# Performance work log

Measured on AMD Instinct MI355X. Metric: run time of the kernel, lower is better.

## Reference

```python
import jax, jax.numpy as jnp
import numpy as np

CH = [344, 352, 686, 679, 1246, 973]  # int(128*3*0.8984), etc.


def binarize(x):
    # sign forward, hardtanh STE backward (standard 1W1A binarization)
    cl = jnp.clip(x, -1.0, 1.0)
    return cl + jax.lax.stop_gradient(jnp.sign(x) - cl)


def bconv(x, w):
    # BinarizeConv2d: conv(sign(x), sign(w)), 3x3, stride 1, pad 1, no bias
    return jax.lax.conv_general_dilated(
        binarize(x), binarize(w), (1, 1), ((1, 1), (1, 1)),
        dimension_numbers=("NCHW", "OIHW", "NCHW"))


def bn(x, p, eps=1e-5):
    # p: [4, C] stacked (gamma, beta, running_mean, running_var), inference BN
    g, b, m, v = p[0], p[1], p[2], p[3]
    scale = (g * jax.lax.rsqrt(v + eps))[None, :, None, None]
    return (x - m[None, :, None, None]) * scale + b[None, :, None, None]


def pool(x):
    return jax.lax.reduce_window(x, -jnp.inf, jax.lax.max,
                                 (1, 1, 2, 2), (1, 1, 2, 2), "VALID")


def htanh(x):
    return jnp.clip(x, -1.0, 1.0)


def setup_inputs() -> dict:
    key = jax.random.key(0)
    ks = jax.random.split(key, 20)
    x = jax.random.normal(ks[0], (256, 3, 32, 32), jnp.float32)
    chs = [3] + CH
    out = {"x": x}
    for i in range(6):
        n = 3 * 3 * chs[i + 1]
        w = jax.random.normal(ks[1 + i], (chs[i + 1], chs[i], 3, 3), jnp.float32) * np.sqrt(2.0 / n).astype(np.float32)
        out[f"w{i}"] = w
        g = jnp.ones((chs[i + 1],), jnp.float32)
        b = jnp.zeros((chs[i + 1],), jnp.float32)
        m = jax.random.normal(ks[7 + i], (chs[i + 1],), jnp.float32) * 0.1
        v = jax.random.uniform(ks[13 + i], (chs[i + 1],), jnp.float32) * 0.5 + 0.5
        out[f"p{i}"] = jnp.stack([g, b, m, v])
    out["fcw"] = jax.random.normal(ks[19], (10, 15568), jnp.float32) * 0.01
    out["fcb"] = jnp.zeros((10,), jnp.float32)
    return out


def reference(x, w0, w1, w2, w3, w4, w5, p0, p1, p2, p3, p4, p5, fcw, fcb):
    x = htanh(bn(bconv(x, w0), p0))          # [B,344,32,32]
    x = htanh(bn(pool(bconv(x, w1)), p1))    # [B,352,16,16]
    x = htanh(bn(bconv(x, w2), p2))          # [B,686,16,16]
    x = htanh(bn(pool(bconv(x, w3)), p3))    # [B,679,8,8]
    x = htanh(bn(bconv(x, w4), p4))          # [B,1246,8,8]
    x = htanh(bn(pool(bconv(x, w5)), p5))    # [B,973,4,4]
    x = x.reshape(x.shape[0], -1)            # [B,15568]
    return binarize(x) @ binarize(fcw).T + fcb
```

## Files before the change

kernel.cpp:

```cpp
#include <hip/hip_runtime.h>
#include <stdint.h>

typedef unsigned long long u64;
typedef int v4i  __attribute__((ext_vector_type(4)));
typedef int v8i  __attribute__((ext_vector_type(8)));
typedef float v16f __attribute__((ext_vector_type(16)));

static __device__ __forceinline__ v16f mfma_fp4(v4i a, v4i b, v16f c) {
    v8i A, B;
    A[0] = a[0]; A[1] = a[1]; A[2] = a[2]; A[3] = a[3];
    A[4] = a[0]; A[5] = a[1]; A[6] = a[2]; A[7] = a[3];
    B[0] = b[0]; B[1] = b[1]; B[2] = b[2]; B[3] = b[3];
    B[4] = b[0]; B[5] = b[1]; B[6] = b[2]; B[7] = b[3];
    return __builtin_amdgcn_mfma_scale_f32_32x32x64_f8f6f4(
        A, B, c, 4, 4, 0, 0x7F7F7F7F, 0, 0x7F7F7F7F);
}

static __device__ __forceinline__ void gload_lds16(const void* g, void* l) {
    __builtin_amdgcn_global_load_lds(
        (const __attribute__((address_space(1))) unsigned int*)g,
        (__attribute__((address_space(3))) unsigned int*)l, 16, 0, 0);
}

__global__ void pack_input_kernel(const float* __restrict__ x, u64* __restrict__ a0)
{
    int idx = blockIdx.x * blockDim.x + threadIdx.x;
    if (idx >= 256 * 1024) return;
    int b = idx >> 10, pix = idx & 1023;
    const float* xp = x + (size_t)b * 3072 + pix;
    u64 wd = 0;
    if (xp[0]    > 0.f) wd |= 1ull;
    if (xp[1024] > 0.f) wd |= 2ull;
    if (xp[2048] > 0.f) wd |= 4ull;
    a0[idx] = wd;
}

__global__ void pack_w_fp4(const float* __restrict__ w, unsigned* __restrict__ wb,
                           int O, int C, int KWIN, int OCG)
{
    int idx = blockIdx.x * blockDim.x + threadIdx.x;
    int total = 9 * KWIN * OCG * 64;
    if (idx >= total) return;
    int lane = idx & 63;
    int rest = idx >> 6;
    int og = rest % OCG; rest /= OCG;
    int c64 = rest % KWIN; int t = rest / KWIN;
    int oc = og * 32 + (lane & 31);
    int h = lane >> 5;
    unsigned out[4];
#pragma unroll
    for (int d = 0; d < 4; ++d) {
        unsigned dw = 0;
#pragma unroll
        for (int j = 0; j < 8; ++j) {
            int c = c64 * 64 + h * 32 + d * 8 + ((j >> 1) + (j & 1) * 4);
            unsigned nib = 0;
            if (oc < O && c < C)
                nib = (w[(size_t)(oc * C + c) * 9 + t] > 0.f) ? 0x2u : 0xAu;
            dw |= nib << (4 * j);
        }
        out[d] = dw;
    }
    *(v4i*)(wb + (size_t)idx * 4) = *(v4i*)out;
}

__global__ void pack_bn_kernel(const float* __restrict__ p, float* __restrict__ sa,
                               float* __restrict__ sb, int C)
{
    int i = blockIdx.x * blockDim.x + threadIdx.x;
    if (i >= C) return;
    float g = p[i], b = p[C + i], m = p[2 * C + i], v = p[3 * C + i];
    float s = g * rsqrtf(v + 1e-5f);
    sa[i] = s;
    sb[i] = fmaf(-m, s, b);
}

__global__ void pack_fc_kernel(const float* __restrict__ fcw, u64* __restrict__ wfc)
{
    int idx = blockIdx.x * blockDim.x + threadIdx.x;
    if (idx >= 10 * 256) return;
    int w = idx & 15;
    int p = (idx >> 4) & 15;
    int k = idx >> 8;
    u64 word = 0;
    for (int c2 = 0; c2 < 64; ++c2) {
        int c = w * 64 + c2;
        if (c < 973) {
            if (fcw[(size_t)k * 15568 + c * 16 + p] > 0.f) word |= (1ull << c2);
        }
    }
    wfc[idx] = word;
}

static __device__ __forceinline__ v4i fp4_unpack32(unsigned wh)
{
    v4i r;
#pragma unroll
    for (int d = 0; d < 4; ++d) {
        unsigned b = (wh >> (8 * d)) & 0xffu;
        unsigned lo = ((b & 0xFu) * 0x00204081u) & 0x01010101u;
        unsigned hi = ((b >> 4)   * 0x00204081u) & 0x01010101u;
        unsigned spread = lo | (hi << 4);
        r[d] = (int)(0xAAAAAAAAu - (spread << 3));
    }
    return r;
}

template <int H, int W, int TH, int TW, int NIMG, int KWIN, int OCG_T, int OCW,
          int COUT, bool POOL>
__global__ __launch_bounds__(256, 2)
void conv_v6f(const u64* __restrict__ act, const char* __restrict__ wb,
              const float* __restrict__ sA, const float* __restrict__ sB,
              u64* __restrict__ outp)
{
    constexpr int CW = TW + 2;
    constexpr int CELLS_I = (TH + 2) * CW;
    constexpr int CELLS = NIMG * CELLS_I;
    constexpr int PLANE = CELLS * 16;
    constexpr int BSZ = 18432;
    __shared__ __attribute__((aligned(16))) char smem[BSZ + 2 * PLANE];

    const int tid  = threadIdx.x;
    const int lane = tid & 63;
    const int wm   = tid >> 6;
    const int h    = lane >> 5;
    const int m    = lane & 31;

    int b0i, y0;
    if constexpr (NIMG == 1) {
        b0i = blockIdx.x >> 1;
        y0 = (blockIdx.x & 1) * TH;
    } else {
        b0i = blockIdx.x * NIMG;
        y0 = 0;
    }

    const int ocg0 = blockIdx.y * 2;
    const int gw   = blockIdx.y;

    int aoff[4];
#pragma unroll
    for (int ag = 0; ag < 4; ++ag) {
        int p = wm * 128 + ag * 32 + m;
        int img = p / (TH * TW);
        int pp = p % (TH * TW);
        aoff[ag] = ((img * CELLS_I + (pp / TW) * CW + (pp % TW)) << 4) + h * PLANE;
    }

    v16f acc[4][2];
#pragma unroll
    for (int ag = 0; ag < 4; ++ag)
#pragma unroll
        for (int o = 0; o < 2; ++o)
#pragma unroll
            for (int i = 0; i < 16; ++i) acc[ag][o][i] = 0.0f;

#pragma unroll 1
    for (int c64 = 0; c64 < KWIN; ++c64) {
        for (int u = wm; u < 18; u += 4) {
            int og = u & 1, t = u >> 1;
            const char* gp = wb + ((size_t)((t * KWIN + c64) * OCG_T + ocg0 + og)) * 1024
                             + lane * 16;
            gload_lds16(gp, smem + u * 1024);
        }
        for (int cell = tid; cell < CELLS; cell += 256) {
            int img, c2;
            if constexpr (NIMG == 1) { img = 0; c2 = cell; }
            else { img = cell / CELLS_I; c2 = cell % CELLS_I; }
            int cy = c2 / CW, cx = c2 % CW;
            int gy = y0 + cy - 1, gx = cx - 1;
            char* dst = smem + BSZ + cell * 16;
            if ((unsigned)gy < (unsigned)H && (unsigned)gx < (unsigned)W) {
                u64 wd = act[((size_t)(b0i + img) * H * W + (size_t)gy * W + gx) * KWIN + c64];
                *(v4i*)dst           = fp4_unpack32((unsigned)wd);
                *(v4i*)(dst + PLANE) = fp4_unpack32((unsigned)(wd >> 32));
            } else {
                v4i z = {0, 0, 0, 0};
                *(v4i*)dst           = z;
                *(v4i*)(dst + PLANE) = z;
            }
        }
        __syncthreads();

#pragma unroll
        for (int t = 0; t < 9; ++t) {
            const int aimm = BSZ + (((t / 3) * CW) + (t % 3)) * 16;
            v4i b0 = *(const v4i*)(smem + (t * 2 + 0) * 1024 + lane * 16);
            v4i b1 = *(const v4i*)(smem + (t * 2 + 1) * 1024 + lane * 16);
            v4i a0 = *(const v4i*)(smem + aoff[0] + aimm);
            v4i a1 = *(const v4i*)(smem + aoff[1] + aimm);
            v4i a2 = *(const v4i*)(smem + aoff[2] + aimm);
            v4i a3 = *(const v4i*)(smem + aoff[3] + aimm);
            acc[0][0] = mfma_fp4(a0, b0, acc[0][0]);
            acc[1][0] = mfma_fp4(a1, b0, acc[1][0]);
            acc[2][0] = mfma_fp4(a2, b0, acc[2][0]);
            acc[3][0] = mfma_fp4(a3, b0, acc[3][0]);
            acc[0][1] = mfma_fp4(a0, b1, acc[0][1]);
            acc[1][1] = mfma_fp4(a1, b1, acc[1][1]);
            acc[2][1] = mfma_fp4(a2, b1, acc[2][1]);
            acc[3][1] = mfma_fp4(a3, b1, acc[3][1]);
        }
        __syncthreads();
    }

    const int ocA = ocg0 * 32 + m;
    const int ocB = ocA + 32;
    const float fa0 = sA[ocA < COUT ? ocA : 0], fb0 = sB[ocA < COUT ? ocA : 0];
    const float fa1 = sA[ocB < COUT ? ocB : 0], fb1 = sB[ocB < COUT ? ocB : 0];

#pragma unroll
    for (int ag = 0; ag < 4; ++ag) {
        if constexpr (POOL && TW == 32) {
            if (ag & 1) continue;
#pragma unroll
            for (int gi = 0; gi < 8; ++gi) {
                const int g = gi * 2;
                float v0 = fmaxf(fmaxf(acc[ag][0][g], acc[ag][0][g ^ 1]),
                                 fmaxf(acc[ag + 1][0][g], acc[ag + 1][0][g ^ 1]));
                float v1 = fmaxf(fmaxf(acc[ag][1][g], acc[ag][1][g ^ 1]),
                                 fmaxf(acc[ag + 1][1][g], acc[ag + 1][1][g ^ 1]));
                u64 bal0 = __ballot((ocA < COUT) && (fmaf(v0, fa0, fb0) > 0.f));
                u64 bal1 = __ballot((ocB < COUT) && (fmaf(v1, fa1, fb1) > 0.f));
                u64 w_lo = (bal0 & 0xffffffffull) | (bal1 << 32);
                u64 w_hi = (bal0 >> 32) | (bal1 & 0xffffffff00000000ull);
                int pyo  = wm * 2 + (ag >> 1);
                int pxo0 = ((g & 3) >> 1) + 4 * (g >> 2);
                size_t rowb = ((size_t)b0i * (H / 2) + (y0 / 2 + pyo)) * (W / 2);
                if (lane == (ag >> 1) * 16 + gi * 2)
                    outp[(rowb + pxo0) * OCW + gw] = w_lo;
                else if (lane == (ag >> 1) * 16 + gi * 2 + 1)
                    outp[(rowb + pxo0 + 2) * OCW + gw] = w_hi;
            }
        } else if constexpr (POOL) {
#pragma unroll
            for (int gi = 0; gi < 4; ++gi) {
                const int g = gi * 2;
                float v0 = fmaxf(fmaxf(acc[ag][0][g], acc[ag][0][g ^ 1]),
                                 fmaxf(acc[ag][0][g ^ 8], acc[ag][0][(g ^ 8) | 1]));
                float v1 = fmaxf(fmaxf(acc[ag][1][g], acc[ag][1][g ^ 1]),
                                 fmaxf(acc[ag][1][g ^ 8], acc[ag][1][(g ^ 8) | 1]));
                u64 bal0 = __ballot((ocA < COUT) && (fmaf(v0, fa0, fb0) > 0.f));
                u64 bal1 = __ballot((ocB < COUT) && (fmaf(v1, fa1, fb1) > 0.f));
                u64 w_lo = (bal0 & 0xffffffffull) | (bal1 << 32);
                u64 w_hi = (bal0 >> 32) | (bal1 & 0xffffffff00000000ull);
                int img  = wm >> 1;
                int pyo  = (wm & 1) * 4 + ag;
                int pxo0 = ((g >> 1) & 1) | (((g >> 2) & 1) << 2);
                size_t rowb = ((size_t)(b0i + img) * (TH / 2) + pyo) * (TW / 2);
                if (lane == (ag * 4 + gi) * 2)
                    outp[(rowb + pxo0) * OCW + gw] = w_lo;
                else if (lane == (ag * 4 + gi) * 2 + 1)
                    outp[(rowb + pxo0 + 2) * OCW + gw] = w_hi;
            }
        } else {
#pragma unroll
            for (int reg = 0; reg < 16; ++reg) {
                u64 bal0 = __ballot((ocA < COUT) && (fmaf(acc[ag][0][reg], fa0, fb0) > 0.f));
                u64 bal1 = __ballot((ocB < COUT) && (fmaf(acc[ag][1][reg], fa1, fb1) > 0.f));
                u64 w_lo = (bal0 & 0xffffffffull) | (bal1 << 32);
                u64 w_hi = (bal0 >> 32) | (bal1 & 0xffffffff00000000ull);
                int row  = (reg & 3) + 8 * (reg >> 2);
                int p_lo = wm * 128 + ag * 32 + row;
                int p_hi = p_lo + 4;
                if (lane == reg * 2) {
                    int img, py, px;
                    if constexpr (TW == 32) { img = 0; py = p_lo >> 5; px = p_lo & 31; }
                    else { img = p_lo >> 8; py = (p_lo >> 4) & 15; px = p_lo & 15; }
                    outp[(((size_t)(b0i + img) * H + (y0 + py)) * W + px) * OCW + gw] = w_lo;
                } else if (lane == reg * 2 + 1) {
                    int img, py, px;
                    if constexpr (TW == 32) { img = 0; py = p_hi >> 5; px = p_hi & 31; }
                    else { img = p_hi >> 8; py = (p_hi >> 4) & 15; px = p_hi & 15; }
                    outp[(((size_t)(b0i + img) * H + (y0 + py)) * W + px) * OCW + gw] = w_hi;
                }
            }
        }
    }
}

template <int KWIN, int OCG, int OCW, int COUT, bool POOL>
__global__ __launch_bounds__(256, 3)
void conv_m8f(const u64* __restrict__ act, const char* __restrict__ wb,
              const float* __restrict__ sA, const float* __restrict__ sB,
              u64* __restrict__ outp)
{
    constexpr int CELLS = 100;
    constexpr int PLANE = CELLS * 16;
    constexpr int IMG = 2 * PLANE;
    __shared__ __attribute__((aligned(16))) char smem[4 * IMG];

    const int tid  = threadIdx.x;
    const int lane = tid & 63;
    const int wave = tid >> 6;
    const int h    = lane >> 5;
    const int m    = lane & 31;

    const int b = blockIdx.x * 4 + wave;
    const int ocg0 = blockIdx.y * 2;
    const int gw = blockIdx.y;

    int aoff[2];
#pragma unroll
    for (int ph = 0; ph < 2; ++ph) {
        int p = ph * 32 + m;
        aoff[ph] = wave * IMG + ((p >> 3) * 10 + (p & 7)) * 16 + h * PLANE;
    }

    v16f acc[2][2];
#pragma unroll
    for (int a = 0; a < 2; ++a)
#pragma unroll
        for (int o = 0; o < 2; ++o)
#pragma unroll
            for (int i = 0; i < 16; ++i) acc[a][o][i] = 0.0f;

    const u64* actb = act + (size_t)b * (64 * KWIN);

    v4i b0n, b1n;
    {
        const v4i* pn = (const v4i*)(wb + ((size_t)ocg0) * 1024) + lane;
        b0n = pn[0]; b1n = pn[64];
    }

#pragma unroll 1
    for (int c64 = 0; c64 < KWIN; ++c64) {
        for (int cell = lane; cell < CELLS; cell += 64) {
            int cy = cell / 10, cx = cell % 10;
            int gy = cy - 1, gx = cx - 1;
            char* dst = smem + wave * IMG + cell * 16;
            if ((unsigned)gy < 8u && (unsigned)gx < 8u) {
                u64 wd = actb[((size_t)gy * 8 + gx) * KWIN + c64];
                *(v4i*)dst           = fp4_unpack32((unsigned)wd);
                *(v4i*)(dst + PLANE) = fp4_unpack32((unsigned)(wd >> 32));
            } else {
                v4i z = {0, 0, 0, 0};
                *(v4i*)dst           = z;
                *(v4i*)(dst + PLANE) = z;
            }
        }
        __syncthreads();

#pragma unroll
        for (int t = 0; t < 9; ++t) {
            v4i b0 = b0n, b1 = b1n;
            {
                const int tn = (t + 1) % 9;
                const int cn = (t == 8) ? (c64 + 1) : c64;
                const v4i* pn = (const v4i*)(wb + ((size_t)((tn * KWIN + cn) * OCG + ocg0)) * 1024) + lane;
                b0n = pn[0]; b1n = pn[64];
            }
            const int toff = ((t / 3) * 10 + (t % 3)) * 16;
            v4i a0 = *(const v4i*)(smem + aoff[0] + toff);
            v4i a1 = *(const v4i*)(smem + aoff[1] + toff);
            acc[0][0] = mfma_fp4(a0, b0, acc[0][0]);
            acc[1][0] = mfma_fp4(a1, b0, acc[1][0]);
            acc[0][1] = mfma_fp4(a0, b1, acc[0][1]);
            acc[1][1] = mfma_fp4(a1, b1, acc[1][1]);
        }
        __syncthreads();
    }

    const int ocA = ocg0 * 32 + m;
    const int ocB = ocA + 32;
    const float fa0 = sA[ocA < COUT ? ocA : 0], fb0 = sB[ocA < COUT ? ocA : 0];
    const float fa1 = sA[ocB < COUT ? ocB : 0], fb1 = sB[ocB < COUT ? ocB : 0];

#pragma unroll
    for (int ph = 0; ph < 2; ++ph) {
        if constexpr (POOL) {
#pragma unroll
            for (int gi = 0; gi < 4; ++gi) {
                const int g = (gi & 1) * 2 + (gi >> 1) * 8;
                float v0 = fmaxf(fmaxf(acc[ph][0][g], acc[ph][0][g ^ 1]),
                                 fmaxf(acc[ph][0][g ^ 4], acc[ph][0][(g ^ 4) | 1]));
                float v1 = fmaxf(fmaxf(acc[ph][1][g], acc[ph][1][g ^ 1]),
                                 fmaxf(acc[ph][1][g ^ 4], acc[ph][1][(g ^ 4) | 1]));
                u64 bal0 = __ballot((ocA < COUT) && (fmaf(v0, fa0, fb0) > 0.f));
                u64 bal1 = __ballot((ocB < COUT) && (fmaf(v1, fa1, fb1) > 0.f));
                u64 w_lo = (bal0 & 0xffffffffull) | (bal1 << 32);
                u64 w_hi = (bal0 >> 32) | (bal1 & 0xffffffff00000000ull);
                int pyo  = ph * 2 + ((g >> 3) & 1);
                int pxo0 = (g >> 1) & 1;
                int pxo1 = pxo0 | 2;
                size_t rowb = ((size_t)b * 4 + pyo) * 4;
                if (lane == (ph * 4 + gi) * 2)
                    outp[(rowb + pxo0) * OCW + gw] = w_lo;
                else if (lane == (ph * 4 + gi) * 2 + 1)
                    outp[(rowb + pxo1) * OCW + gw] = w_hi;
            }
        } else {
#pragma unroll
            for (int reg = 0; reg < 16; ++reg) {
                u64 bal0 = __ballot((ocA < COUT) && (fmaf(acc[ph][0][reg], fa0, fb0) > 0.f));
                u64 bal1 = __ballot((ocB < COUT) && (fmaf(acc[ph][1][reg], fa1, fb1) > 0.f));
                u64 w_lo = (bal0 & 0xffffffffull) | (bal1 << 32);
                u64 w_hi = (bal0 >> 32) | (bal1 & 0xffffffff00000000ull);
                int row  = (reg & 3) + 8 * (reg >> 2);
                int p_lo = ph * 32 + row;
                int p_hi = p_lo + 4;
                if (lane == reg * 2)
                    outp[(((size_t)b * 8 + (p_lo >> 3)) * 8 + (p_lo & 7)) * OCW + gw] = w_lo;
                else if (lane == reg * 2 + 1)
                    outp[(((size_t)b * 8 + (p_hi >> 3)) * 8 + (p_hi & 7)) * OCW + gw] = w_hi;
            }
        }
    }
}

__global__ void fc_kernel(const u64* __restrict__ a6, const u64* __restrict__ wfc,
                          const float* __restrict__ fcb, float* __restrict__ out)
{
    int idx = blockIdx.x * blockDim.x + threadIdx.x;
    if (idx >= 2560) return;
    int k = idx % 10, b = idx / 10;
    const u64* ap = a6 + (size_t)b * 256;
    const u64* wq = wfc + (size_t)k * 256;
    int pop = 0;
#pragma unroll 8
    for (int q = 0; q < 256; ++q) pop += __popcll(ap[q] ^ wq[q]);
    out[idx] = (float)(15568 - 2 * pop) + fcb[k];
}

extern "C" void kernel_launch(void* const* d_in, const int* in_sizes, int n_in,
                              void* d_out, int out_size, void* d_ws, size_t ws_size,
                              hipStream_t stream)
{
    const float* x   = (const float*)d_in[0];
    const float* w0  = (const float*)d_in[1];
    const float* p0  = (const float*)d_in[2];
    const float* w1  = (const float*)d_in[3];
    const float* p1  = (const float*)d_in[4];
    const float* w2  = (const float*)d_in[5];
    const float* p2  = (const float*)d_in[6];
    const float* w3  = (const float*)d_in[7];
    const float* p3  = (const float*)d_in[8];
    const float* w4  = (const float*)d_in[9];
    const float* p4  = (const float*)d_in[10];
    const float* w5  = (const float*)d_in[11];
    const float* p5  = (const float*)d_in[12];
    const float* fcw = (const float*)d_in[13];
    const float* fcb = (const float*)d_in[14];
    float* out = (float*)d_out;

    u64* WS = (u64*)d_ws;
    u64* A0 = WS;
    u64* A1 = A0 + 262144;
    u64* A2 = A1 + 1572864;
    u64* A3 = A2 + 393216;
    u64* A4 = A3 + 720896;
    u64* A5 = A4 + 180224;
    u64* A6 = A5 + 327680;
    u64* WFp = A6 + 65536;
    char* WB0 = (char*)(WFp + 2560);
    char* WB1 = WB0 + 110592;
    char* WB2 = WB1 + 663552;
    char* WB3 = WB2 + 1327104;
    char* WB4 = WB3 + 2433024;
    char* WB5 = WB4 + 4055040;
    float* SA0 = (float*)(WB5 + 5898240);
    float* SB0 = SA0 + 1280;
    float* SA1 = SB0 + 1280;
    float* SB1 = SA1 + 1280;
    float* SA2 = SB1 + 1280;
    float* SB2 = SA2 + 1280;
    float* SA3 = SB2 + 1280;
    float* SB3 = SA3 + 1280;
    float* SA4 = SB3 + 1280;
    float* SB4 = SA4 + 1280;
    float* SA5 = SB4 + 1280;
    float* SB5 = SA5 + 1280;

    pack_input_kernel<<<1024, 256, 0, stream>>>(x, A0);
    pack_w_fp4<<<(9 * 1 * 12 * 64 + 255) / 256, 256, 0, stream>>>(w0, (unsigned*)WB0, 344, 3, 1, 12);
    pack_w_fp4<<<(9 * 6 * 12 * 64 + 255) / 256, 256, 0, stream>>>(w1, (unsigned*)WB1, 352, 344, 6, 12);
    pack_w_fp4<<<(9 * 6 * 24 * 64 + 255) / 256, 256, 0, stream>>>(w2, (unsigned*)WB2, 686, 352, 6, 24);
    pack_w_fp4<<<(9 * 11 * 24 * 64 + 255) / 256, 256, 0, stream>>>(w3, (unsigned*)WB3, 679, 686, 11, 24);
    pack_w_fp4<<<(9 * 11 * 40 * 64 + 255) / 256, 256, 0, stream>>>(w4, (unsigned*)WB4, 1246, 679, 11, 40);
    pack_w_fp4<<<(9 * 20 * 32 * 64 + 255) / 256, 256, 0, stream>>>(w5, (unsigned*)WB5, 973, 1246, 20, 32);
    pack_bn_kernel<<<2, 256, 0, stream>>>(p0, SA0, SB0, 344);
    pack_bn_kernel<<<2, 256, 0, stream>>>(p1, SA1, SB1, 352);
    pack_bn_kernel<<<3, 256, 0, stream>>>(p2, SA2, SB2, 686);
    pack_bn_kernel<<<3, 256, 0, stream>>>(p3, SA3, SB3, 679);
    pack_bn_kernel<<<5, 256, 0, stream>>>(p4, SA4, SB4, 1246);
    pack_bn_kernel<<<4, 256, 0, stream>>>(p5, SA5, SB5, 973);
    pack_fc_kernel<<<10, 256, 0, stream>>>(fcw, WFp);

    conv_v6f<32, 32, 16, 32, 1,  1, 12,  6, 344, false>
        <<<dim3(512, 6), 256, 0, stream>>>(A0, WB0, SA0, SB0, A1);
    conv_v6f<32, 32, 16, 32, 1,  6, 12,  6, 352, true>
        <<<dim3(512, 6), 256, 0, stream>>>(A1, WB1, SA1, SB1, A2);
    conv_v6f<16, 16, 16, 16, 2,  6, 24, 11, 686, false>
        <<<dim3(128, 11), 256, 0, stream>>>(A2, WB2, SA2, SB2, A3);
    conv_v6f<16, 16, 16, 16, 2, 11, 24, 11, 679, true>
        <<<dim3(128, 11), 256, 0, stream>>>(A3, WB3, SA3, SB3, A4);
    conv_m8f<11, 40, 20, 1246, false>
        <<<dim3(64, 20), 256, 0, stream>>>(A4, WB4, SA4, SB4, A5);
    conv_m8f<20, 32, 16, 973, true>
        <<<dim3(64, 16), 256, 0, stream>>>(A5, WB5, SA5, SB5, A6);

    fc_kernel<<<10, 256, 0, stream>>>(A6, WFp, fcb, out);
}
```

Baseline: 971.3 us.

## Double-buffer conv tiles and prefetch next channel chunk during MFMA loop

The main conv kernel now keeps two LDS buffers. During the MFMA loop over the current 64-channel chunk it prefetches the next chunk's weights, via global_load_lds, and its activation words into registers. Cell addresses and zero padding are computed once up front, and one of the two block barriers per iteration is removed. The 8x8 per-wave kernel drops its block barriers and uses wave-local lgkmcnt waits, with register prefetch of the next chunk's activations. The cost is twice the LDS for the main kernel, which may lower occupancy, and a risk of wave-level races in the per-wave kernel.

After: 3.088 ms. +218.0%, slower.

```diff
diff --git a/kernel.cpp b/kernel.cpp
--- a/kernel.cpp
+++ b/kernel.cpp
@@ -118,7 +118,10 @@
     constexpr int CELLS = NIMG * CELLS_I;
     constexpr int PLANE = CELLS * 16;
     constexpr int BSZ = 18432;
-    __shared__ __attribute__((aligned(16))) char smem[BSZ + 2 * PLANE];
+    constexpr int BUF = BSZ + 2 * PLANE;
+    constexpr int NBUF = (KWIN > 1) ? 2 : 1;
+    constexpr int NCELL = (CELLS + 255) / 256;
+    __shared__ __attribute__((aligned(16))) char smem[NBUF * BUF];
 
     const int tid  = threadIdx.x;
     const int lane = tid & 63;
@@ -147,50 +150,98 @@
         aoff[ag] = ((img * CELLS_I + (pp / TW) * CW + (pp % TW)) << 4) + h * PLANE;
     }
 
-    v16f acc[4][2];
-#pragma unroll
-    for (int ag = 0; ag < 4; ++ag)
-#pragma unroll
-        for (int o = 0; o < 2; ++o)
-#pragma unroll
-            for (int i = 0; i < 16; ++i) acc[ag][o][i] = 0.0f;
-
-#pragma unroll 1
-    for (int c64 = 0; c64 < KWIN; ++c64) {
-        for (int u = wm; u < 18; u += 4) {
-            int og = u & 1, t = u >> 1;
-            const char* gp = wb + ((size_t)((t * KWIN + c64) * OCG_T + ocg0 + og)) * 1024
-                             + lane * 16;
-            gload_lds16(gp, smem + u * 1024);
-        }
-        for (int cell = tid; cell < CELLS; cell += 256) {
+    const u64* cp[NCELL];
+    int  coff[NCELL];
+    bool cval[NCELL];
+#pragma unroll
+    for (int i = 0; i < NCELL; ++i) {
+        cval[i] = false; cp[i] = act; coff[i] = 0;
+        int cell = tid + i * 256;
+        if (cell < CELLS) {
             int img, c2;
             if constexpr (NIMG == 1) { img = 0; c2 = cell; }
             else { img = cell / CELLS_I; c2 = cell % CELLS_I; }
             int cy = c2 / CW, cx = c2 % CW;
             int gy = y0 + cy - 1, gx = cx - 1;
-            char* dst = smem + BSZ + cell * 16;
+            coff[i] = cell * 16;
             if ((unsigned)gy < (unsigned)H && (unsigned)gx < (unsigned)W) {
-                u64 wd = act[((size_t)(b0i + img) * H * W + (size_t)gy * W + gx) * KWIN + c64];
-                *(v4i*)dst           = fp4_unpack32((unsigned)wd);
-                *(v4i*)(dst + PLANE) = fp4_unpack32((unsigned)(wd >> 32));
+                cval[i] = true;
+                cp[i] = act + ((size_t)(b0i + img) * H * W + (size_t)gy * W + gx) * KWIN;
             } else {
                 v4i z = {0, 0, 0, 0};
-                *(v4i*)dst           = z;
-                *(v4i*)(dst + PLANE) = z;
-            }
-        }
-        __syncthreads();
+                *(v4i*)(smem + BSZ + cell * 16)         = z;
+                *(v4i*)(smem + BSZ + cell * 16 + PLANE) = z;
+                if constexpr (NBUF == 2) {
+                    *(v4i*)(smem + BUF + BSZ + cell * 16)         = z;
+                    *(v4i*)(smem + BUF + BSZ + cell * 16 + PLANE) = z;
+                }
+            }
+        }
+    }
+
+    const char* bsrc[5];
+#pragma unroll
+    for (int k = 0; k < 5; ++k) {
+        const int u = wm + 4 * k;
+        if (u < 18) {
+            const int og = u & 1, t = u >> 1;
+            bsrc[k] = wb + ((size_t)(t * KWIN * OCG_T + ocg0 + og)) * 1024 + lane * 16;
+            gload_lds16(bsrc[k], smem + u * 1024);
+        } else {
+            bsrc[k] = wb;
+        }
+    }
+    {
+        u64 wd0[NCELL];
+#pragma unroll
+        for (int i = 0; i < NCELL; ++i) wd0[i] = cval[i] ? cp[i][0] : 0;
+#pragma unroll
+        for (int i = 0; i < NCELL; ++i) if (cval[i]) {
+            char* dst = smem + BSZ + coff[i];
+            *(v4i*)dst           = fp4_unpack32((unsigned)wd0[i]);
+            *(v4i*)(dst + PLANE) = fp4_unpack32((unsigned)(wd0[i] >> 32));
+        }
+    }
+    __syncthreads();
+
+    v16f acc[4][2];
+#pragma unroll
+    for (int ag = 0; ag < 4; ++ag)
+#pragma unroll
+        for (int o = 0; o < 2; ++o)
+#pragma unroll
+            for (int i = 0; i < 16; ++i) acc[ag][o][i] = 0.0f;
+
+#pragma unroll 1
+    for (int c64 = 0; c64 < KWIN; ++c64) {
+        const int cur = c64 & 1;
+        const char* sb = smem + cur * BUF;
+        char* nb = smem + ((NBUF == 2) ? ((cur ^ 1) * BUF) : 0);
+        const bool more = (c64 + 1 < KWIN);
+
+        u64 wd[NCELL];
+        if (more) {
+#pragma unroll
+            for (int i = 0; i < NCELL; ++i) wd[i] = cval[i] ? cp[i][c64 + 1] : 0;
+#pragma unroll
+            for (int k = 0; k < 5; ++k) {
+                const int u = wm + 4 * k;
+                if (u < 18) {
+                    bsrc[k] += (size_t)OCG_T * 1024;
+                    gload_lds16(bsrc[k], nb + u * 1024);
+                }
+            }
+        }
 
 #pragma unroll
         for (int t = 0; t < 9; ++t) {
             const int aimm = BSZ + (((t / 3) * CW) + (t % 3)) * 16;
-            v4i b0 = *(const v4i*)(smem + (t * 2 + 0) * 1024 + lane * 16);
-            v4i b1 = *(const v4i*)(smem + (t * 2 + 1) * 1024 + lane * 16);
-            v4i a0 = *(const v4i*)(smem + aoff[0] + aimm);
-            v4i a1 = *(const v4i*)(smem + aoff[1] + aimm);
-            v4i a2 = *(const v4i*)(smem + aoff[2] + aimm);
-            v4i a3 = *(const v4i*)(smem + aoff[3] + aimm);
+            v4i b0 = *(const v4i*)(sb + (t * 2 + 0) * 1024 + lane * 16);
+            v4i b1 = *(const v4i*)(sb + (t * 2 + 1) * 1024 + lane * 16);
+            v4i a0 = *(const v4i*)(sb + aoff[0] + aimm);
+            v4i a1 = *(const v4i*)(sb + aoff[1] + aimm);
+            v4i a2 = *(const v4i*)(sb + aoff[2] + aimm);
+            v4i a3 = *(const v4i*)(sb + aoff[3] + aimm);
             acc[0][0] = mfma_fp4(a0, b0, acc[0][0]);
             acc[1][0] = mfma_fp4(a1, b0, acc[1][0]);
             acc[2][0] = mfma_fp4(a2, b0, acc[2][0]);
@@ -200,7 +251,16 @@
             acc[2][1] = mfma_fp4(a2, b1, acc[2][1]);
             acc[3][1] = mfma_fp4(a3, b1, acc[3][1]);
         }
-        __syncthreads();
+
+        if (more) {
+#pragma unroll
+            for (int i = 0; i < NCELL; ++i) if (cval[i]) {
+                char* dst = nb + BSZ + coff[i];
+                *(v4i*)dst           = fp4_unpack32((unsigned)wd[i]);
+                *(v4i*)(dst + PLANE) = fp4_unpack32((unsigned)(wd[i] >> 32));
+            }
+            __syncthreads();
+        }
     }
 
     const int ocA = ocg0 * 32 + m;
@@ -306,6 +366,38 @@
         aoff[ph] = wave * IMG + ((p >> 3) * 10 + (p & 7)) * 16 + h * PLANE;
     }
 
+    const u64* actb = act + (size_t)b * (64 * KWIN);
+
+    const u64* cp0 = actb; int co0; bool cv0;
+    const u64* cp1 = actb; int co1 = 0; bool cv1 = false;
+    {
+        int cy = lane / 10, cx = lane % 10;
+        int gy = cy - 1, gx = cx - 1;
+        co0 = wave * IMG + lane * 16;
+        cv0 = ((unsigned)gy < 8u && (unsigned)gx < 8u);
+        if (cv0) {
+            cp0 = actb + ((size_t)(gy * 8 + gx)) * KWIN;
+        } else {
+            v4i z = {0, 0, 0, 0};
+            *(v4i*)(smem + co0)         = z;
+            *(v4i*)(smem + co0 + PLANE) = z;
+        }
+        int cell1 = lane + 64;
+        if (cell1 < CELLS) {
+            int cy1 = cell1 / 10, cx1 = cell1 % 10;
+            int gy1 = cy1 - 1, gx1 = cx1 - 1;
+            co1 = wave * IMG + cell1 * 16;
+            cv1 = ((unsigned)gy1 < 8u && (unsigned)gx1 < 8u);
+            if (cv1) {
+                cp1 = actb + ((size_t)(gy1 * 8 + gx1)) * KWIN;
+            } else {
+                v4i z = {0, 0, 0, 0};
+                *(v4i*)(smem + co1)         = z;
+                *(v4i*)(smem + co1 + PLANE) = z;
+            }
+        }
+    }
+
     v16f acc[2][2];
 #pragma unroll
     for (int a = 0; a < 2; ++a)
@@ -313,8 +405,6 @@
         for (int o = 0; o < 2; ++o)
 #pragma unroll
             for (int i = 0; i < 16; ++i) acc[a][o][i] = 0.0f;
-
-    const u64* actb = act + (size_t)b * (64 * KWIN);
 
     v4i b0n, b1n;
     {
@@ -322,23 +412,31 @@
         b0n = pn[0]; b1n = pn[64];
     }
 
+    {
+        u64 w0 = cv0 ? cp0[0] : 0;
+        u64 w1 = cv1 ? cp1[0] : 0;
+        if (cv0) {
+            char* d = smem + co0;
+            *(v4i*)d           = fp4_unpack32((unsigned)w0);
+            *(v4i*)(d + PLANE) = fp4_unpack32((unsigned)(w0 >> 32));
+        }
+        if (cv1) {
+            char* d = smem + co1;
+            *(v4i*)d           = fp4_unpack32((unsigned)w1);
+            *(v4i*)(d + PLANE) = fp4_unpack32((unsigned)(w1 >> 32));
+        }
+    }
+    asm volatile("s_waitcnt lgkmcnt(0)" ::: "memory");
+    __builtin_amdgcn_sched_barrier(0);
+
 #pragma unroll 1
     for (int c64 = 0; c64 < KWIN; ++c64) {
-        for (int cell = lane; cell < CELLS; cell += 64) {
-            int cy = cell / 10, cx = cell % 10;
-            int gy = cy - 1, gx = cx - 1;
-            char* dst = smem + wave * IMG + cell * 16;
-            if ((unsigned)gy < 8u && (unsigned)gx < 8u) {
-                u64 wd = actb[((size_t)gy * 8 + gx) * KWIN + c64];
-                *(v4i*)dst           = fp4_unpack32((unsigned)wd);
-                *(v4i*)(dst + PLANE) = fp4_unpack32((unsigned)(wd >> 32));
-            } else {
-                v4i z = {0, 0, 0, 0};
-                *(v4i*)dst           = z;
-                *(v4i*)(dst + PLANE) = z;
-            }
-        }
-        __syncthreads();
+        const bool more = (c64 + 1 < KWIN);
+        u64 nw0 = 0, nw1 = 0;
+        if (more) {
+            nw0 = cv0 ? cp0[c64 + 1] : 0;
+            nw1 = cv1 ? cp1[c64 + 1] : 0;
+        }
 
 #pragma unroll
         for (int t = 0; t < 9; ++t) {
@@ -357,7 +455,23 @@
             acc[0][1] = mfma_fp4(a0, b1, acc[0][1]);
             acc[1][1] = mfma_fp4(a1, b1, acc[1][1]);
         }
-        __syncthreads();
+
+        asm volatile("s_waitcnt lgkmcnt(0)" ::: "memory");
+        __builtin_amdgcn_sched_barrier(0);
+        if (more) {
+            if (cv0) {
+                char* d = smem + co0;
+                *(v4i*)d           = fp4_unpack32((unsigned)nw0);
+                *(v4i*)(d + PLANE) = fp4_unpack32((unsigned)(nw0 >> 32));
+            }
+            if (cv1) {
+                char* d = smem + co1;
+                *(v4i*)d           = fp4_unpack32((unsigned)nw1);
+                *(v4i*)(d + PLANE) = fp4_unpack32((unsigned)(nw1 >> 32));
+            }
+            asm volatile("s_waitcnt lgkmcnt(0)" ::: "memory");
+            __builtin_amdgcn_sched_barrier(0);
+        }
     }
 
     const int ocA = ocg0 * 32 + m;
```

## Double-buffer weight tiles and switch activations to channel-word-major layout

Applied to the files above, without the earlier changes.

Conv kernels now load the next channel window's weight tiles into a second LDS buffer asynchronously while MFMAs run on the current one. Per-thread cell coordinates are precomputed once, and halo zeros are written only at the start. The packed activation layout changes from pixel-major with interleaved channel words to channel-word-major planes, so each stage read and output write is contiguous per word group; the FC kernel is updated to index the new layout. The cost is extra LDS for the second weight buffer, which may lower occupancy, plus a redundant duplicated A load in the inner loop.

After: 1.840 ms. +89.4%, slower.

```diff
diff --git a/kernel.cpp b/kernel.cpp
--- a/kernel.cpp
+++ b/kernel.cpp
@@ -118,7 +118,13 @@
     constexpr int CELLS = NIMG * CELLS_I;
     constexpr int PLANE = CELLS * 16;
     constexpr int BSZ = 18432;
-    __shared__ __attribute__((aligned(16))) char smem[BSZ + 2 * PLANE];
+    constexpr int NBB = (KWIN > 1) ? 2 : 1;
+    constexpr int AOFS = NBB * BSZ;
+    constexpr int NCELL = (CELLS + 255) / 256;
+    constexpr size_t NPX  = (size_t)256 * H * W;
+    constexpr size_t NPXO = POOL ? ((size_t)256 * (H / 2) * (W / 2))
+                                 : ((size_t)256 * H * W);
+    __shared__ __attribute__((aligned(16))) char smem[AOFS + 2 * PLANE];
 
     const int tid  = threadIdx.x;
     const int lane = tid & 63;
@@ -147,50 +153,79 @@
         aoff[ag] = ((img * CELLS_I + (pp / TW) * CW + (pp % TW)) << 4) + h * PLANE;
     }
 
-    v16f acc[4][2];
-#pragma unroll
-    for (int ag = 0; ag < 4; ++ag)
-#pragma unroll
-        for (int o = 0; o < 2; ++o)
-#pragma unroll
-            for (int i = 0; i < 16; ++i) acc[ag][o][i] = 0.0f;
-
-#pragma unroll 1
-    for (int c64 = 0; c64 < KWIN; ++c64) {
-        for (int u = wm; u < 18; u += 4) {
-            int og = u & 1, t = u >> 1;
-            const char* gp = wb + ((size_t)((t * KWIN + c64) * OCG_T + ocg0 + og)) * 1024
-                             + lane * 16;
-            gload_lds16(gp, smem + u * 1024);
-        }
-        for (int cell = tid; cell < CELLS; cell += 256) {
+    int cpx[NCELL];
+    int coff[NCELL];
+#pragma unroll
+    for (int i = 0; i < NCELL; ++i) {
+        cpx[i] = -1; coff[i] = 0;
+        int cell = tid + i * 256;
+        if (cell < CELLS) {
             int img, c2;
             if constexpr (NIMG == 1) { img = 0; c2 = cell; }
             else { img = cell / CELLS_I; c2 = cell % CELLS_I; }
             int cy = c2 / CW, cx = c2 % CW;
             int gy = y0 + cy - 1, gx = cx - 1;
-            char* dst = smem + BSZ + cell * 16;
+            coff[i] = AOFS + cell * 16;
             if ((unsigned)gy < (unsigned)H && (unsigned)gx < (unsigned)W) {
-                u64 wd = act[((size_t)(b0i + img) * H * W + (size_t)gy * W + gx) * KWIN + c64];
-                *(v4i*)dst           = fp4_unpack32((unsigned)wd);
-                *(v4i*)(dst + PLANE) = fp4_unpack32((unsigned)(wd >> 32));
+                cpx[i] = (b0i + img) * (H * W) + gy * W + gx;
             } else {
                 v4i z = {0, 0, 0, 0};
-                *(v4i*)dst           = z;
-                *(v4i*)(dst + PLANE) = z;
-            }
-        }
-        __syncthreads();
+                *(v4i*)(smem + coff[i])         = z;
+                *(v4i*)(smem + coff[i] + PLANE) = z;
+            }
+        }
+    }
+
+    auto stageB = [&](int c) {
+        char* bb = smem + ((NBB == 2) ? ((c & 1) * BSZ) : 0);
+        for (int u = wm; u < 18; u += 4) {
+            int og = u & 1, t = u >> 1;
+            const char* gp = wb + ((size_t)((t * KWIN + c) * OCG_T + ocg0 + og)) * 1024
+                             + lane * 16;
+            gload_lds16(gp, bb + u * 1024);
+        }
+    };
+    auto stageA = [&](int c) {
+        u64 wd[NCELL];
+#pragma unroll
+        for (int i = 0; i < NCELL; ++i)
+            wd[i] = (cpx[i] >= 0) ? act[(size_t)c * NPX + cpx[i]] : 0;
+#pragma unroll
+        for (int i = 0; i < NCELL; ++i) if (cpx[i] >= 0) {
+            char* dst = smem + coff[i];
+            *(v4i*)dst           = fp4_unpack32((unsigned)wd[i]);
+            *(v4i*)(dst + PLANE) = fp4_unpack32((unsigned)(wd[i] >> 32));
+        }
+    };
+
+    stageB(0);
+    stageA(0);
+    __syncthreads();
+
+    v16f acc[4][2];
+#pragma unroll
+    for (int ag = 0; ag < 4; ++ag)
+#pragma unroll
+        for (int o = 0; o < 2; ++o)
+#pragma unroll
+            for (int i = 0; i < 16; ++i) acc[ag][o][i] = 0.0f;
+
+#pragma unroll 1
+    for (int c64 = 0; c64 < KWIN; ++c64) {
+        if (c64 + 1 < KWIN) stageB(c64 + 1);
+
+        const char* sb = smem + ((NBB == 2) ? ((c64 & 1) * BSZ) : 0);
 
 #pragma unroll
         for (int t = 0; t < 9; ++t) {
-            const int aimm = BSZ + (((t / 3) * CW) + (t % 3)) * 16;
-            v4i b0 = *(const v4i*)(smem + (t * 2 + 0) * 1024 + lane * 16);
-            v4i b1 = *(const v4i*)(smem + (t * 2 + 1) * 1024 + lane * 16);
-            v4i a0 = *(const v4i*)(smem + aoff[0] + aimm);
+            const int aimm = AOFS + (((t / 3) * CW) + (t % 3)) * 16;
+            v4i b0 = *(const v4i*)(sb + (t * 2 + 0) * 1024 + lane * 16);
+            v4i b1 = *(const v4i*)(sb + (t * 2 + 1) * 1024 + lane * 16);
+            v4i a0 = *(const v4i*)(smem + aoff[0] + aimm - AOFS + AOFS);
             v4i a1 = *(const v4i*)(smem + aoff[1] + aimm);
             v4i a2 = *(const v4i*)(smem + aoff[2] + aimm);
             v4i a3 = *(const v4i*)(smem + aoff[3] + aimm);
+            a0 = *(const v4i*)(smem + aoff[0] + aimm);
             acc[0][0] = mfma_fp4(a0, b0, acc[0][0]);
             acc[1][0] = mfma_fp4(a1, b0, acc[1][0]);
             acc[2][0] = mfma_fp4(a2, b0, acc[2][0]);
@@ -200,13 +235,19 @@
             acc[2][1] = mfma_fp4(a2, b1, acc[2][1]);
             acc[3][1] = mfma_fp4(a3, b1, acc[3][1]);
         }
-        __syncthreads();
+
+        if (c64 + 1 < KWIN) {
+            __syncthreads();
+            stageA(c64 + 1);
+            __syncthreads();
+        }
     }
 
     const int ocA = ocg0 * 32 + m;
     const int ocB = ocA + 32;
     const float fa0 = sA[ocA < COUT ? ocA : 0], fb0 = sB[ocA < COUT ? ocA : 0];
     const float fa1 = sA[ocB < COUT ? ocB : 0], fb1 = sB[ocB < COUT ? ocB : 0];
+    u64* outg = outp + (size_t)gw * NPXO;
 
 #pragma unroll
     for (int ag = 0; ag < 4; ++ag) {
@@ -227,9 +268,9 @@
                 int pxo0 = ((g & 3) >> 1) + 4 * (g >> 2);
                 size_t rowb = ((size_t)b0i * (H / 2) + (y0 / 2 + pyo)) * (W / 2);
                 if (lane == (ag >> 1) * 16 + gi * 2)
-                    outp[(rowb + pxo0) * OCW + gw] = w_lo;
+                    outg[rowb + pxo0] = w_lo;
                 else if (lane == (ag >> 1) * 16 + gi * 2 + 1)
-                    outp[(rowb + pxo0 + 2) * OCW + gw] = w_hi;
+                    outg[rowb + pxo0 + 2] = w_hi;
             }
         } else if constexpr (POOL) {
 #pragma unroll
@@ -248,9 +289,9 @@
                 int pxo0 = ((g >> 1) & 1) | (((g >> 2) & 1) << 2);
                 size_t rowb = ((size_t)(b0i + img) * (TH / 2) + pyo) * (TW / 2);
                 if (lane == (ag * 4 + gi) * 2)
-                    outp[(rowb + pxo0) * OCW + gw] = w_lo;
+                    outg[rowb + pxo0] = w_lo;
                 else if (lane == (ag * 4 + gi) * 2 + 1)
-                    outp[(rowb + pxo0 + 2) * OCW + gw] = w_hi;
+                    outg[rowb + pxo0 + 2] = w_hi;
             }
         } else {
 #pragma unroll
@@ -266,12 +307,12 @@
                     int img, py, px;
                     if constexpr (TW == 32) { img = 0; py = p_lo >> 5; px = p_lo & 31; }
                     else { img = p_lo >> 8; py = (p_lo >> 4) & 15; px = p_lo & 15; }
-                    outp[(((size_t)(b0i + img) * H + (y0 + py)) * W + px) * OCW + gw] = w_lo;
+                    outg[((size_t)(b0i + img) * H + (y0 + py)) * W + px] = w_lo;
                 } else if (lane == reg * 2 + 1) {
                     int img, py, px;
                     if constexpr (TW == 32) { img = 0; py = p_hi >> 5; px = p_hi & 31; }
                     else { img = p_hi >> 8; py = (p_hi >> 4) & 15; px = p_hi & 15; }
-                    outp[(((size_t)(b0i + img) * H + (y0 + py)) * W + px) * OCW + gw] = w_hi;
+                    outg[((size_t)(b0i + img) * H + (y0 + py)) * W + px] = w_hi;
                 }
             }
         }
@@ -287,6 +328,8 @@
     constexpr int CELLS = 100;
     constexpr int PLANE = CELLS * 16;
     constexpr int IMG = 2 * PLANE;
+    constexpr int NPX8 = 16384;
+    constexpr size_t NPXO = POOL ? 4096 : 16384;
     __shared__ __attribute__((aligned(16))) char smem[4 * IMG];
 
     const int tid  = threadIdx.x;
@@ -314,7 +357,7 @@
 #pragma unroll
             for (int i = 0; i < 16; ++i) acc[a][o][i] = 0.0f;
 
-    const u64* actb = act + (size_t)b * (64 * KWIN);
+    const u64* actb = act + (size_t)b * 64;
 
     v4i b0n, b1n;
     {
@@ -329,7 +372,7 @@
             int gy = cy - 1, gx = cx - 1;
             char* dst = smem + wave * IMG + cell * 16;
             if ((unsigned)gy < 8u && (unsigned)gx < 8u) {
-                u64 wd = actb[((size_t)gy * 8 + gx) * KWIN + c64];
+                u64 wd = actb[(size_t)c64 * NPX8 + (gy * 8 + gx)];
                 *(v4i*)dst           = fp4_unpack32((unsigned)wd);
                 *(v4i*)(dst + PLANE) = fp4_unpack32((unsigned)(wd >> 32));
             } else {
@@ -364,6 +407,7 @@
     const int ocB = ocA + 32;
     const float fa0 = sA[ocA < COUT ? ocA : 0], fb0 = sB[ocA < COUT ? ocA : 0];
     const float fa1 = sA[ocB < COUT ? ocB : 0], fb1 = sB[ocB < COUT ? ocB : 0];
+    u64* outg = outp + (size_t)gw * NPXO;
 
 #pragma unroll
     for (int ph = 0; ph < 2; ++ph) {
@@ -384,9 +428,9 @@
                 int pxo1 = pxo0 | 2;
                 size_t rowb = ((size_t)b * 4 + pyo) * 4;
                 if (lane == (ph * 4 + gi) * 2)
-                    outp[(rowb + pxo0) * OCW + gw] = w_lo;
+                    outg[rowb + pxo0] = w_lo;
                 else if (lane == (ph * 4 + gi) * 2 + 1)
-                    outp[(rowb + pxo1) * OCW + gw] = w_hi;
+                    outg[rowb + pxo1] = w_hi;
             }
         } else {
 #pragma unroll
@@ -399,9 +443,9 @@
                 int p_lo = ph * 32 + row;
                 int p_hi = p_lo + 4;
                 if (lane == reg * 2)
-                    outp[(((size_t)b * 8 + (p_lo >> 3)) * 8 + (p_lo & 7)) * OCW + gw] = w_lo;
+                    outg[((size_t)b * 8 + (p_lo >> 3)) * 8 + (p_lo & 7)] = w_lo;
                 else if (lane == reg * 2 + 1)
-                    outp[(((size_t)b * 8 + (p_hi >> 3)) * 8 + (p_hi & 7)) * OCW + gw] = w_hi;
+                    outg[((size_t)b * 8 + (p_hi >> 3)) * 8 + (p_hi & 7)] = w_hi;
             }
         }
     }
@@ -413,11 +457,13 @@
     int idx = blockIdx.x * blockDim.x + threadIdx.x;
     if (idx >= 2560) return;
     int k = idx % 10, b = idx / 10;
-    const u64* ap = a6 + (size_t)b * 256;
     const u64* wq = wfc + (size_t)k * 256;
     int pop = 0;
 #pragma unroll 8
-    for (int q = 0; q < 256; ++q) pop += __popcll(ap[q] ^ wq[q]);
+    for (int q = 0; q < 256; ++q) {
+        int w = q & 15, p = q >> 4;
+        pop += __popcll(a6[(size_t)w * 4096 + b * 16 + p] ^ wq[q]);
+    }
     out[idx] = (float)(15568 - 2 * pop) + fcb[k];
 }
 
```

## Switch packed activation layout to channel-group-major planes

Applied to the files above, without the earlier changes.

Stores binarized activations as [channel-word][pixel] planes instead of [pixel][channel-word] interleaved. Conv kernels now read contiguous pixels for a given 64-channel word and write per-word planes, which should coalesce both the global loads in the tile staging and the scattered ballot stores. The FC kernel is adapted to gather from the new layout, making its reads strided across planes.

Result: faster. 938.0 us (-3.4%).

```diff
diff --git a/kernel.cpp b/kernel.cpp
--- a/kernel.cpp
+++ b/kernel.cpp
@@ -118,6 +118,9 @@
     constexpr int CELLS = NIMG * CELLS_I;
     constexpr int PLANE = CELLS * 16;
     constexpr int BSZ = 18432;
+    constexpr size_t NPX  = (size_t)256 * H * W;
+    constexpr size_t NPXO = POOL ? ((size_t)256 * (H / 2) * (W / 2))
+                                 : ((size_t)256 * H * W);
     __shared__ __attribute__((aligned(16))) char smem[BSZ + 2 * PLANE];
 
     const int tid  = threadIdx.x;
@@ -171,7 +174,8 @@
             int gy = y0 + cy - 1, gx = cx - 1;
             char* dst = smem + BSZ + cell * 16;
             if ((unsigned)gy < (unsigned)H && (unsigned)gx < (unsigned)W) {
-                u64 wd = act[((size_t)(b0i + img) * H * W + (size_t)gy * W + gx) * KWIN + c64];
+                u64 wd = act[(size_t)c64 * NPX
+                             + (size_t)(b0i + img) * (H * W) + gy * W + gx];
                 *(v4i*)dst           = fp4_unpack32((unsigned)wd);
                 *(v4i*)(dst + PLANE) = fp4_unpack32((unsigned)(wd >> 32));
             } else {
@@ -207,6 +211,7 @@
     const int ocB = ocA + 32;
     const float fa0 = sA[ocA < COUT ? ocA : 0], fb0 = sB[ocA < COUT ? ocA : 0];
     const float fa1 = sA[ocB < COUT ? ocB : 0], fb1 = sB[ocB < COUT ? ocB : 0];
+    u64* outg = outp + (size_t)gw * NPXO;
 
 #pragma unroll
     for (int ag = 0; ag < 4; ++ag) {
@@ -227,9 +232,9 @@
                 int pxo0 = ((g & 3) >> 1) + 4 * (g >> 2);
                 size_t rowb = ((size_t)b0i * (H / 2) + (y0 / 2 + pyo)) * (W / 2);
                 if (lane == (ag >> 1) * 16 + gi * 2)
-                    outp[(rowb + pxo0) * OCW + gw] = w_lo;
+                    outg[rowb + pxo0] = w_lo;
                 else if (lane == (ag >> 1) * 16 + gi * 2 + 1)
-                    outp[(rowb + pxo0 + 2) * OCW + gw] = w_hi;
+                    outg[rowb + pxo0 + 2] = w_hi;
             }
         } else if constexpr (POOL) {
 #pragma unroll
@@ -248,9 +253,9 @@
                 int pxo0 = ((g >> 1) & 1) | (((g >> 2) & 1) << 2);
                 size_t rowb = ((size_t)(b0i + img) * (TH / 2) + pyo) * (TW / 2);
                 if (lane == (ag * 4 + gi) * 2)
-                    outp[(rowb + pxo0) * OCW + gw] = w_lo;
+                    outg[rowb + pxo0] = w_lo;
                 else if (lane == (ag * 4 + gi) * 2 + 1)
-                    outp[(rowb + pxo0 + 2) * OCW + gw] = w_hi;
+                    outg[rowb + pxo0 + 2] = w_hi;
             }
         } else {
 #pragma unroll
@@ -266,12 +271,12 @@
                     int img, py, px;
                     if constexpr (TW == 32) { img = 0; py = p_lo >> 5; px = p_lo & 31; }
                     else { img = p_lo >> 8; py = (p_lo >> 4) & 15; px = p_lo & 15; }
-                    outp[(((size_t)(b0i + img) * H + (y0 + py)) * W + px) * OCW + gw] = w_lo;
+                    outg[((size_t)(b0i + img) * H + (y0 + py)) * W + px] = w_lo;
                 } else if (lane == reg * 2 + 1) {
                     int img, py, px;
                     if constexpr (TW == 32) { img = 0; py = p_hi >> 5; px = p_hi & 31; }
                     else { img = p_hi >> 8; py = (p_hi >> 4) & 15; px = p_hi & 15; }
-                    outp[(((size_t)(b0i + img) * H + (y0 + py)) * W + px) * OCW + gw] = w_hi;
+                    outg[((size_t)(b0i + img) * H + (y0 + py)) * W + px] = w_hi;
                 }
             }
         }
@@ -287,6 +292,8 @@
     constexpr int CELLS = 100;
     constexpr int PLANE = CELLS * 16;
     constexpr int IMG = 2 * PLANE;
+    constexpr int NPX8 = 16384;
+    constexpr size_t NPXO = POOL ? 4096 : 16384;
     __shared__ __attribute__((aligned(16))) char smem[4 * IMG];
 
     const int tid  = threadIdx.x;
@@ -314,7 +321,7 @@
 #pragma unroll
             for (int i = 0; i < 16; ++i) acc[a][o][i] = 0.0f;
 
-    const u64* actb = act + (size_t)b * (64 * KWIN);
+    const u64* actb = act + (size_t)b * 64;
 
     v4i b0n, b1n;
     {
@@ -329,7 +336,7 @@
             int gy = cy - 1, gx = cx - 1;
             char* dst = smem + wave * IMG + cell * 16;
             if ((unsigned)gy < 8u && (unsigned)gx < 8u) {
-                u64 wd = actb[((size_t)gy * 8 + gx) * KWIN + c64];
+                u64 wd = actb[(size_t)c64 * NPX8 + (gy * 8 + gx)];
                 *(v4i*)dst           = fp4_unpack32((unsigned)wd);
                 *(v4i*)(dst + PLANE) = fp4_unpack32((unsigned)(wd >> 32));
             } else {
@@ -364,6 +371,7 @@
     const int ocB = ocA + 32;
     const float fa0 = sA[ocA < COUT ? ocA : 0], fb0 = sB[ocA < COUT ? ocA : 0];
     const float fa1 = sA[ocB < COUT ? ocB : 0], fb1 = sB[ocB < COUT ? ocB : 0];
+    u64* outg = outp + (size_t)gw * NPXO;
 
 #pragma unroll
     for (int ph = 0; ph < 2; ++ph) {
@@ -384,9 +392,9 @@
                 int pxo1 = pxo0 | 2;
                 size_t rowb = ((size_t)b * 4 + pyo) * 4;
                 if (lane == (ph * 4 + gi) * 2)
-                    outp[(rowb + pxo0) * OCW + gw] = w_lo;
+                    outg[rowb + pxo0] = w_lo;
                 else if (lane == (ph * 4 + gi) * 2 + 1)
-                    outp[(rowb + pxo1) * OCW + gw] = w_hi;
+                    outg[rowb + pxo1] = w_hi;
             }
         } else {
 #pragma unroll
@@ -399,9 +407,9 @@
                 int p_lo = ph * 32 + row;
                 int p_hi = p_lo + 4;
                 if (lane == reg * 2)
-                    outp[(((size_t)b * 8 + (p_lo >> 3)) * 8 + (p_lo & 7)) * OCW + gw] = w_lo;
+                    outg[((size_t)b * 8 + (p_lo >> 3)) * 8 + (p_lo & 7)] = w_lo;
                 else if (lane == reg * 2 + 1)
-                    outp[(((size_t)b * 8 + (p_hi >> 3)) * 8 + (p_hi & 7)) * OCW + gw] = w_hi;
+                    outg[((size_t)b * 8 + (p_hi >> 3)) * 8 + (p_hi & 7)] = w_hi;
             }
         }
     }
@@ -413,11 +421,13 @@
     int idx = blockIdx.x * blockDim.x + threadIdx.x;
     if (idx >= 2560) return;
     int k = idx % 10, b = idx / 10;
-    const u64* ap = a6 + (size_t)b * 256;
     const u64* wq = wfc + (size_t)k * 256;
     int pop = 0;
 #pragma unroll 8
-    for (int q = 0; q < 256; ++q) pop += __popcll(ap[q] ^ wq[q]);
+    for (int q = 0; q < 256; ++q) {
+        int w = q & 15, p = q >> 4;
+        pop += __popcll(a6[(size_t)w * 4096 + b * 16 + p] ^ wq[q]);
+    }
     out[idx] = (float)(15568 - 2 * pop) + fcb[k];
 }
 
```
